# Kernel optimization log

Measured on AMD Instinct MI355X. Metric: run time of the kernel, lower is better.

The kernel has to match this reference:

```python
import jax, jax.numpy as jnp
import numpy as np
from jax.ops import segment_sum

N, E, F_IN, G, C = 20000, 640000, 128, 64, 2


def setup_inputs() -> dict:
    key = jax.random.key(0)
    ks = jax.random.split(key, 16)
    g = lambda k, s: (jax.random.normal(k, s, jnp.float32) * 0.05)
    z = lambda s: jnp.zeros(s, jnp.float32)
    inp = {
        'x': jax.random.normal(ks[0], (N, F_IN), jnp.float32),
        'edge_index': jax.random.randint(ks[1], (2, E), 0, N),
        'batch': jnp.sort(jax.random.randint(ks[2], (N,), 0, G)),
        'w1': g(ks[3], (F_IN, 64)), 'b1': z((64,)),
        'w2': g(ks[4], (64, 64)), 'b2': z((64,)),
        'w3': g(ks[5], (64, 128)), 'b3': z((128,)),
        'w4': g(ks[6], (128, 256)), 'b4': z((256,)),
        'lstm_wih': g(ks[7], (512, 256)), 'lstm_whh': g(ks[8], (512, 128)),
        'lstm_bih': z((512,)), 'lstm_bhh': z((512,)),
        'attn_in_w': g(ks[9], (384, 128)), 'attn_in_b': z((384,)),
        'attn_out_w': g(ks[10], (128, 128)), 'attn_out_b': z((128,)),
        'lin1_w': g(ks[11], (64, 128)), 'lin1_b': z((64,)),
        'lin2_w': g(ks[12], (C, 64)), 'lin2_b': z((C,)),
    }
    return inp


def _gcn(x, src, dst, norm, w, b):
    # PyG GCNConv: h = x @ W; out[dst] += norm_e * h[src]; + bias
    h = x @ w
    msg = h[src] * norm[:, None]
    return segment_sum(msg, dst, num_segments=N) + b


def forward(x, edge_index, batch, w1, b1, w2, b2, w3, b3, w4, b4,
            lstm_wih, lstm_whh, lstm_bih, lstm_bhh,
            attn_in_w, attn_in_b, attn_out_w, attn_out_b,
            lin1_w, lin1_b, lin2_w, lin2_b):
    # ---- GCN normalization with self-loops (shared across layers) ----
    loop = jnp.arange(N)
    src = jnp.concatenate([edge_index[0], loop])
    dst = jnp.concatenate([edge_index[1], loop])
    deg = segment_sum(jnp.ones_like(src, jnp.float32), dst, num_segments=N)
    dinv = jnp.where(deg > 0, jax.lax.rsqrt(deg), 0.0)
    norm = dinv[src] * dinv[dst]

    h = jax.nn.relu(_gcn(x, src, dst, norm, w1, b1))   # [N,64]  (dropout = eval no-op)
    h = jax.nn.relu(_gcn(h, src, dst, norm, w2, b2))   # [N,64]
    h = jax.nn.relu(_gcn(h, src, dst, norm, w3, b3))   # [N,128]
    h = jax.nn.relu(_gcn(h, src, dst, norm, w4, b4))   # [N,256]

    # ---- LSTM over the node sequence (batch 1, seq N), PyTorch gate order i,f,g,o ----
    xg = h @ lstm_wih.T + (lstm_bih + lstm_bhh)        # [N,512] precomputed input gates

    def step(carry, xg_t):
        hh, cc = carry
        gates = xg_t + lstm_whh @ hh                    # [512]
        i, f, gg, o = jnp.split(gates, 4)
        i, f, o = jax.nn.sigmoid(i), jax.nn.sigmoid(f), jax.nn.sigmoid(o)
        cc = f * cc + i * jnp.tanh(gg)
        hh = o * jnp.tanh(cc)
        return (hh, cc), hh

    init = (jnp.zeros(128, h.dtype), jnp.zeros(128, h.dtype))
    _, hs = jax.lax.scan(step, init, xg)               # [N,128]

    # ---- MultiheadAttention: input (L=1, B=N, E=128); softmax over length-1 seq ----
    qkv = hs @ attn_in_w.T + attn_in_b                 # [N,384]
    q, k, v = jnp.split(qkv, 3, axis=-1)
    qh = q.reshape(N, 8, 16); kh = k.reshape(N, 8, 16); vh = v.reshape(N, 8, 16)
    scores = jnp.sum(qh * kh, -1, keepdims=True) / 4.0  # [N,8,1], key dim = 1
    a = jax.nn.softmax(scores, axis=-1)                 # == 1 (single key)
    ctx = (a * vh).reshape(N, 128)
    attn = ctx @ attn_out_w.T + attn_out_b             # [N,128]

    # ---- global mean pool over graphs ----
    sums = segment_sum(attn, batch, num_segments=G)    # [G,128]
    cnt = segment_sum(jnp.ones(N, attn.dtype), batch, num_segments=G)
    pooled = sums / jnp.maximum(cnt, 1.0)[:, None]

    z1 = jax.nn.relu(pooled @ lin1_w.T + lin1_b)
    logits = z1 @ lin2_w.T + lin2_b                    # [G,C]
    return jax.nn.log_softmax(logits, axis=1)


def reference(x, edge_index, batch, w1, b1, w2, b2, w3, b3, w4, b4,
              lstm_wih, lstm_whh, lstm_bih, lstm_bhh,
              attn_in_w, attn_in_b, attn_out_w, attn_out_b,
              lin1_w, lin1_b, lin2_w, lin2_b):
    return forward(x, edge_index, batch, w1, b1, w2, b2, w3, b3, w4, b4,
                   lstm_wih, lstm_whh, lstm_bih, lstm_bhh,
                   attn_in_w, attn_in_b, attn_out_w, attn_out_b,
                   lin1_w, lin1_b, lin2_w, lin2_b)
```

## Files before the change

kernel.cpp:

```cpp
#include <hip/hip_runtime.h>
#include <cstdint>
#include <cstddef>

#define N_NODES 20000
#define N_EDGES 640000
#define N_GRAPH 64

typedef __attribute__((ext_vector_type(8))) short bf16x8;
typedef __attribute__((ext_vector_type(4))) float f32x4;

__device__ __forceinline__ float sigmoidf_(float x) {
    return 1.0f / (1.0f + __expf(-x));
}
__device__ __forceinline__ float tanhf_(float x) {
    float xc = fminf(fmaxf(x, -9.0f), 9.0f);
    float e = __expf(2.0f * xc);
    return (e - 1.0f) / (e + 1.0f);
}
__device__ __forceinline__ unsigned short f2bf_(float x) {
    unsigned int u = __builtin_bit_cast(unsigned int, x);
    return (unsigned short)((u + 0x7fffu + ((u >> 16) & 1u)) >> 16);
}

__global__ void count_kernel(const int* __restrict__ dst, int* __restrict__ cnt, int e) {
    int i = blockIdx.x * blockDim.x + threadIdx.x;
    if (i < e) atomicAdd(&cnt[dst[i]], 1);
}

__global__ void scan_kernel(const int* __restrict__ cnt, int* __restrict__ rowstart, int n) {
    __shared__ int buf[1024];
    __shared__ int carry_sh;
    int tid = threadIdx.x;
    if (tid == 0) carry_sh = 0;
    __syncthreads();
    for (int base = 0; base < n; base += 1024) {
        int i = base + tid;
        int v = (i < n) ? cnt[i] : 0;
        buf[tid] = v;
        __syncthreads();
        for (int off = 1; off < 1024; off <<= 1) {
            int t = (tid >= off) ? buf[tid - off] : 0;
            __syncthreads();
            buf[tid] += t;
            __syncthreads();
        }
        int carry = carry_sh;
        if (i < n) rowstart[i] = carry + buf[tid] - v;
        __syncthreads();
        if (tid == 1023) carry_sh = carry + buf[1023];
        __syncthreads();
    }
    if (tid == 0) rowstart[n] = carry_sh;
}

__global__ void dinv_kernel(const int* __restrict__ cnt, float* __restrict__ dinv, int n) {
    int i = blockIdx.x * blockDim.x + threadIdx.x;
    if (i < n) dinv[i] = rsqrtf((float)cnt[i] + 1.0f);
}

__global__ void fill_kernel(const int* __restrict__ src, const int* __restrict__ dst,
                            const int* __restrict__ rowstart, int* __restrict__ cursor,
                            int* __restrict__ csr_src, int e) {
    int i = blockIdx.x * blockDim.x + threadIdx.x;
    if (i < e) {
        int d = dst[i];
        int pos = rowstart[d] + atomicAdd(&cursor[d], 1);
        csr_src[pos] = src[i];
    }
}

template <bool BT, bool RELU, bool BIAS>
__global__ void gemm_kernel(const float* __restrict__ A, const float* __restrict__ B,
                            const float* __restrict__ bias, float* __restrict__ C,
                            int M, int K, int F) {
    __shared__ float As[16][65];
    __shared__ float Bs[16][65];
    int bm = blockIdx.x * 64;
    int bn = blockIdx.y * 64;
    int tid = threadIdx.x;
    int tm = (tid >> 4) << 2;
    int tn = (tid & 15) << 2;
    float acc[4][4] = {};
    for (int k0 = 0; k0 < K; k0 += 16) {
        {
            int idx = tid * 4;
            int m = idx >> 4;
            int kk = idx & 15;
            int gm = bm + m;
            float4 v = make_float4(0.f, 0.f, 0.f, 0.f);
            if (gm < M) v = *(const float4*)&A[(size_t)gm * K + k0 + kk];
            As[kk + 0][m] = v.x; As[kk + 1][m] = v.y; As[kk + 2][m] = v.z; As[kk + 3][m] = v.w;
        }
        if (BT) {
            int idx = tid * 4;
            int nn = idx >> 4;
            int kk = idx & 15;
            float4 v = *(const float4*)&B[(size_t)(bn + nn) * K + k0 + kk];
            Bs[kk + 0][nn] = v.x; Bs[kk + 1][nn] = v.y; Bs[kk + 2][nn] = v.z; Bs[kk + 3][nn] = v.w;
        } else {
            int idx = tid * 4;
            int kk = idx >> 6;
            int nn = idx & 63;
            float4 v = *(const float4*)&B[(size_t)(k0 + kk) * F + bn + nn];
            Bs[kk][nn + 0] = v.x; Bs[kk][nn + 1] = v.y; Bs[kk][nn + 2] = v.z; Bs[kk][nn + 3] = v.w;
        }
        __syncthreads();
#pragma unroll
        for (int kk = 0; kk < 16; ++kk) {
            float av[4], bv[4];
#pragma unroll
            for (int i = 0; i < 4; ++i) av[i] = As[kk][tm + i];
#pragma unroll
            for (int j = 0; j < 4; ++j) bv[j] = Bs[kk][tn + j];
#pragma unroll
            for (int i = 0; i < 4; ++i)
#pragma unroll
                for (int j = 0; j < 4; ++j) acc[i][j] += av[i] * bv[j];
        }
        __syncthreads();
    }
#pragma unroll
    for (int i = 0; i < 4; ++i) {
        int gm = bm + tm + i;
        if (gm >= M) continue;
#pragma unroll
        for (int j = 0; j < 4; ++j) {
            float v = acc[i][j];
            if (BIAS) v += bias[bn + tn + j];
            if (RELU) v = fmaxf(v, 0.0f);
            C[(size_t)gm * F + bn + tn + j] = v;
        }
    }
}

__global__ void agg_kernel(const float* __restrict__ H, const int* __restrict__ rowstart,
                           const int* __restrict__ csr_src, const float* __restrict__ dinv,
                           const float* __restrict__ bias, float* __restrict__ OUT, int F) {
    int n = blockIdx.x;
    int f = threadIdx.x;
    float di = dinv[n];
    int s = rowstart[n], e = rowstart[n + 1];
    float acc = di * H[(size_t)n * F + f];
    for (int i = s; i < e; ++i) {
        int src = csr_src[i];
        acc += dinv[src] * H[(size_t)src * F + f];
    }
    OUT[(size_t)n * F + f] = fmaxf(bias[f] + di * acc, 0.0f);
}

__global__ void vadd_kernel(const float* __restrict__ a, const float* __restrict__ b,
                            float* __restrict__ o, int n) {
    int i = blockIdx.x * blockDim.x + threadIdx.x;
    if (i < n) o[i] = a[i] + b[i];
}

__global__ void wprep_kernel(const float* __restrict__ whh, uint4* __restrict__ out) {
    int tau = blockIdx.x * blockDim.x + threadIdx.x;
    if (tau >= 8192) return;
    int l  = tau & 63;
    int f  = (tau >> 6) & 7;
    int w  = tau >> 9;
    int s  = f >> 2, kc = f & 3;
    int grow = 32 * w + 16 * s + (l & 15);
    int kb   = kc * 32 + (l >> 4) * 8;
    const float* src = whh + (size_t)grow * 128 + kb;
    unsigned int h[8];
#pragma unroll
    for (int j = 0; j < 8; ++j) h[j] = f2bf_(src[j]);
    uint4 v;
    v.x = h[0] | (h[1] << 16);
    v.y = h[2] | (h[3] << 16);
    v.z = h[4] | (h[5] << 16);
    v.w = h[6] | (h[7] << 16);
    out[tau] = v;
}

#define REP8(OP) OP(0) OP(1) OP(2) OP(3) OP(4) OP(5) OP(6) OP(7)

__global__ __launch_bounds__(1024)
__attribute__((amdgpu_waves_per_eu(4, 4)))
void lstm_mfma_kernel(const float* __restrict__ xg, const bf16x8* wfr,
                      const int* __restrict__ batch, float* poolsum, int steps) {
    __shared__ __align__(16) unsigned short h_bf[2][128];
    __shared__ __align__(16) float gates_s[512];
    const int t = threadIdx.x;
    const int w = t >> 6;
    const int l = t & 63;
    const int lg = l >> 4;
    const int rbase = 32 * w + 4 * lg;

#define AF(i) bf16x8 af##i = wfr[(size_t)(w * 8 + (i)) * 64 + l]; \
    asm volatile("" : "+v"(af##i));
    REP8(AF)
#undef AF

    if (t < 128) h_bf[0][t] = 0;
    float c = 0.0f, pacc = 0.0f;
    int curb = batch[0];
    f32x4 xc0 = *(const f32x4*)(xg + rbase);
    f32x4 xc1 = *(const f32x4*)(xg + rbase + 16);
    __syncthreads();

    int p = 0;
    for (int n = 0; n < steps; ++n) {
        bf16x8 b0 = *(const bf16x8*)&h_bf[p][ 0 + lg * 8];
        bf16x8 b1 = *(const bf16x8*)&h_bf[p][32 + lg * 8];
        bf16x8 b2 = *(const bf16x8*)&h_bf[p][64 + lg * 8];
        bf16x8 b3 = *(const bf16x8*)&h_bf[p][96 + lg * 8];

        const float* xp = xg + (size_t)((n + 1 < steps) ? n + 1 : n) * 512;
        f32x4 xn0 = *(const f32x4*)(xp + rbase);
        f32x4 xn1 = *(const f32x4*)(xp + rbase + 16);

        f32x4 a0 = xc0, a1 = xc1;
        a0 = __builtin_amdgcn_mfma_f32_16x16x32_bf16(af0, b0, a0, 0, 0, 0);
        a1 = __builtin_amdgcn_mfma_f32_16x16x32_bf16(af4, b0, a1, 0, 0, 0);
        a0 = __builtin_amdgcn_mfma_f32_16x16x32_bf16(af1, b1, a0, 0, 0, 0);
        a1 = __builtin_amdgcn_mfma_f32_16x16x32_bf16(af5, b1, a1, 0, 0, 0);
        a0 = __builtin_amdgcn_mfma_f32_16x16x32_bf16(af2, b2, a0, 0, 0, 0);
        a1 = __builtin_amdgcn_mfma_f32_16x16x32_bf16(af6, b2, a1, 0, 0, 0);
        a0 = __builtin_amdgcn_mfma_f32_16x16x32_bf16(af3, b3, a0, 0, 0, 0);
        a1 = __builtin_amdgcn_mfma_f32_16x16x32_bf16(af7, b3, a1, 0, 0, 0);

        if ((l & 15) == 0) {
            *(f32x4*)&gates_s[rbase]      = a0;
            *(f32x4*)&gates_s[rbase + 16] = a1;
        }
        __syncthreads();

        if (t < 128) {
            float iv = sigmoidf_(gates_s[t]);
            float fv = sigmoidf_(gates_s[t + 128]);
            float gg = tanhf_(gates_s[t + 256]);
            float ov = sigmoidf_(gates_s[t + 384]);
            c = fv * c + iv * gg;
            float hn = ov * tanhf_(c);
            h_bf[p ^ 1][t] = f2bf_(hn);
            int b = batch[n];
            if (b != curb) { poolsum[curb * 128 + t] = pacc; pacc = 0.0f; curb = b; }
            pacc += hn;
        }
        __syncthreads();

        xc0 = xn0; xc1 = xn1; p ^= 1;
    }
    if (t < 128) poolsum[curb * 128 + t] = pacc;
}

__global__ void head_kernel(const float* __restrict__ poolsum, const int* __restrict__ batch,
                            int nn,
                            const float* __restrict__ attn_in_w, const float* __restrict__ attn_in_b,
                            const float* __restrict__ attn_out_w, const float* __restrict__ attn_out_b,
                            const float* __restrict__ l1w, const float* __restrict__ l1b,
                            const float* __restrict__ l2w, const float* __restrict__ l2b,
                            float* __restrict__ out) {
    __shared__ float hbar[128], tv[128], pl[128], z1[64], lg[2];
    int g = blockIdx.x, t = threadIdx.x;
    int lo = 0, hi = nn;
    while (lo < hi) { int m = (lo + hi) >> 1; if (batch[m] < g) lo = m + 1; else hi = m; }
    int s0 = lo;
    lo = 0; hi = nn;
    while (lo < hi) { int m = (lo + hi) >> 1; if (batch[m] <= g) lo = m + 1; else hi = m; }
    int e0 = lo;
    float cntv = fmaxf((float)(e0 - s0), 1.0f);
    hbar[t] = poolsum[g * 128 + t] / cntv;
    __syncthreads();
    float a = attn_in_b[256 + t];
    for (int k = 0; k < 128; ++k) a += attn_in_w[(256 + t) * 128 + k] * hbar[k];
    tv[t] = a;
    __syncthreads();
    float pv = attn_out_b[t];
    for (int k = 0; k < 128; ++k) pv += attn_out_w[t * 128 + k] * tv[k];
    pl[t] = pv;
    __syncthreads();
    if (t < 64) {
        float z = l1b[t];
        for (int k = 0; k < 128; ++k) z += l1w[t * 128 + k] * pl[k];
        z1[t] = fmaxf(z, 0.0f);
    }
    __syncthreads();
    if (t < 2) {
        float lv = l2b[t];
        for (int k = 0; k < 64; ++k) lv += l2w[t * 64 + k] * z1[k];
        lg[t] = lv;
    }
    __syncthreads();
    if (t == 0) {
        float m = fmaxf(lg[0], lg[1]);
        float ls = m + logf(__expf(lg[0] - m) + __expf(lg[1] - m));
        out[g * 2 + 0] = lg[0] - ls;
        out[g * 2 + 1] = lg[1] - ls;
    }
}

extern "C" void kernel_launch(void* const* d_in, const int* in_sizes, int n_in,
                              void* d_out, int out_size, void* d_ws, size_t ws_size,
                              hipStream_t stream) {
    const float* x          = (const float*)d_in[0];
    const int*   ei         = (const int*)d_in[1];
    const int*   batch      = (const int*)d_in[2];
    const float* w1 = (const float*)d_in[3];  const float* b1 = (const float*)d_in[4];
    const float* w2 = (const float*)d_in[5];  const float* b2 = (const float*)d_in[6];
    const float* w3 = (const float*)d_in[7];  const float* b3 = (const float*)d_in[8];
    const float* w4 = (const float*)d_in[9];  const float* b4 = (const float*)d_in[10];
    const float* wih = (const float*)d_in[11]; const float* whh = (const float*)d_in[12];
    const float* bih = (const float*)d_in[13]; const float* bhh = (const float*)d_in[14];
    const float* attn_in_w  = (const float*)d_in[15]; const float* attn_in_b  = (const float*)d_in[16];
    const float* attn_out_w = (const float*)d_in[17]; const float* attn_out_b = (const float*)d_in[18];
    const float* l1w = (const float*)d_in[19]; const float* l1b = (const float*)d_in[20];
    const float* l2w = (const float*)d_in[21]; const float* l2b = (const float*)d_in[22];
    float* out = (float*)d_out;

    char* p = (char*)d_ws;
    auto alloc = [&](size_t bytes) {
        char* r = p;
        p += (bytes + 255) & ~(size_t)255;
        return r;
    };
    int*   cnt      = (int*)alloc((size_t)N_NODES * 4);
    int*   cursor   = (int*)alloc((size_t)N_NODES * 4);
    int*   rowstart = (int*)alloc((size_t)(N_NODES + 1) * 4);
    float* dinv     = (float*)alloc((size_t)N_NODES * 4);
    int*   csr      = (int*)alloc((size_t)N_EDGES * 4);
    float* bsum     = (float*)alloc(512 * 4);
    float* poolsum  = (float*)alloc((size_t)N_GRAPH * 128 * 4);
    uint4* wfrag    = (uint4*)alloc((size_t)8192 * 16);
    float* bufA     = (float*)alloc((size_t)N_NODES * 256 * 4);
    float* bufB     = (float*)alloc((size_t)N_NODES * 256 * 4);
    float* xg       = (float*)alloc((size_t)N_NODES * 512 * 4);

    hipMemsetAsync(cnt, 0, (size_t)N_NODES * 4, stream);
    hipMemsetAsync(cursor, 0, (size_t)N_NODES * 4, stream);
    hipMemsetAsync(poolsum, 0, (size_t)N_GRAPH * 128 * 4, stream);

    const int* srcp = ei;
    const int* dstp = ei + N_EDGES;

    int eb = (N_EDGES + 255) / 256;
    int nb = (N_NODES + 255) / 256;
    count_kernel<<<eb, 256, 0, stream>>>(dstp, cnt, N_EDGES);
    scan_kernel<<<1, 1024, 0, stream>>>(cnt, rowstart, N_NODES);
    dinv_kernel<<<nb, 256, 0, stream>>>(cnt, dinv, N_NODES);
    fill_kernel<<<eb, 256, 0, stream>>>(srcp, dstp, rowstart, cursor, csr, N_EDGES);
    wprep_kernel<<<32, 256, 0, stream>>>(whh, wfrag);

    int mg = (N_NODES + 63) / 64;
    gemm_kernel<false, false, false><<<dim3(mg, 1), 256, 0, stream>>>(x, w1, nullptr, bufA, N_NODES, 128, 64);
    agg_kernel<<<N_NODES, 64, 0, stream>>>(bufA, rowstart, csr, dinv, b1, bufB, 64);
    gemm_kernel<false, false, false><<<dim3(mg, 1), 256, 0, stream>>>(bufB, w2, nullptr, bufA, N_NODES, 64, 64);
    agg_kernel<<<N_NODES, 64, 0, stream>>>(bufA, rowstart, csr, dinv, b2, bufB, 64);
    gemm_kernel<false, false, false><<<dim3(mg, 2), 256, 0, stream>>>(bufB, w3, nullptr, bufA, N_NODES, 64, 128);
    agg_kernel<<<N_NODES, 128, 0, stream>>>(bufA, rowstart, csr, dinv, b3, bufB, 128);
    gemm_kernel<false, false, false><<<dim3(mg, 4), 256, 0, stream>>>(bufB, w4, nullptr, bufA, N_NODES, 128, 256);
    agg_kernel<<<N_NODES, 256, 0, stream>>>(bufA, rowstart, csr, dinv, b4, bufB, 256);

    vadd_kernel<<<2, 256, 0, stream>>>(bih, bhh, bsum, 512);
    gemm_kernel<true, false, true><<<dim3(mg, 8), 256, 0, stream>>>(bufB, wih, bsum, xg, N_NODES, 256, 512);

    lstm_mfma_kernel<<<1, 1024, 0, stream>>>(xg, (const bf16x8*)wfrag, batch, poolsum, N_NODES);

    head_kernel<<<N_GRAPH, 128, 0, stream>>>(poolsum, batch, N_NODES,
                                             attn_in_w, attn_in_b, attn_out_w, attn_out_b,
                                             l1w, l1b, l2w, l2b, out);
}
```

Measured before the change: 15.10 ms.

## Halve LSTM block to 8 waves holding weight fragments in AGPRs via inline asm

The sequential LSTM kernel now runs with 512 threads (8 waves) instead of 1024. Each wave computes 64 gate rows, so it needs four MFMA accumulator chains and 16 weight fragments, which are pinned in accumulation registers with v_accvgpr_write and used by hand-written MFMA asm. The input-gate contribution xg is no longer the MFMA accumulator seed. It is added afterwards by the 128 activation threads, which also prefetch the next step's values. The aim is to cut per-step barrier cost and wave count on the latency-bound recurrence. The risks are manual hazard handling (s_nop padding), clobbered AGPRs the compiler cannot see, and a longer MFMA dependency chain per wave.

```diff
diff --git a/kernel.cpp b/kernel.cpp
--- a/kernel.cpp
+++ b/kernel.cpp
@@ -158,10 +158,10 @@
     int tau = blockIdx.x * blockDim.x + threadIdx.x;
     if (tau >= 8192) return;
     int l  = tau & 63;
-    int f  = (tau >> 6) & 7;
-    int w  = tau >> 9;
+    int f  = (tau >> 6) & 15;
+    int w  = tau >> 10;
     int s  = f >> 2, kc = f & 3;
-    int grow = 32 * w + 16 * s + (l & 15);
+    int grow = 64 * w + 16 * s + (l & 15);
     int kb   = kc * 32 + (l >> 4) * 8;
     const float* src = whh + (size_t)grow * 128 + kb;
     unsigned int h[8];
@@ -175,30 +175,38 @@
     out[tau] = v;
 }
 
-#define REP8(OP) OP(0) OP(1) OP(2) OP(3) OP(4) OP(5) OP(6) OP(7)
-
-__global__ __launch_bounds__(1024)
-__attribute__((amdgpu_waves_per_eu(4, 4)))
-void lstm_mfma_kernel(const float* __restrict__ xg, const bf16x8* wfr,
-                      const int* __restrict__ batch, float* poolsum, int steps) {
+#define SF(i, A0, A1, A2, A3) { \
+    uint4 q = wfr[(size_t)(w * 16 + (i)) * 64 + l]; \
+    asm volatile("v_accvgpr_write_b32 a" #A0 ", %0\n\t" \
+                 "v_accvgpr_write_b32 a" #A1 ", %1\n\t" \
+                 "v_accvgpr_write_b32 a" #A2 ", %2\n\t" \
+                 "v_accvgpr_write_b32 a" #A3 ", %3" \
+                 :: "v"(q.x), "v"(q.y), "v"(q.z), "v"(q.w) \
+                 : "a" #A0, "a" #A1, "a" #A2, "a" #A3); }
+
+__global__ __launch_bounds__(512)
+void lstm_mfma_kernel(const float* __restrict__ xg, const uint4* __restrict__ wfr,
+                      const int* __restrict__ batch, float* __restrict__ poolsum, int steps) {
     __shared__ __align__(16) unsigned short h_bf[2][128];
     __shared__ __align__(16) float gates_s[512];
     const int t = threadIdx.x;
     const int w = t >> 6;
     const int l = t & 63;
     const int lg = l >> 4;
-    const int rbase = 32 * w + 4 * lg;
-
-#define AF(i) bf16x8 af##i = wfr[(size_t)(w * 8 + (i)) * 64 + l]; \
-    asm volatile("" : "+v"(af##i));
-    REP8(AF)
-#undef AF
+
+    SF(0, 0, 1, 2, 3)     SF(1, 4, 5, 6, 7)     SF(2, 8, 9, 10, 11)    SF(3, 12, 13, 14, 15)
+    SF(4, 16, 17, 18, 19) SF(5, 20, 21, 22, 23) SF(6, 24, 25, 26, 27)  SF(7, 28, 29, 30, 31)
+    SF(8, 32, 33, 34, 35) SF(9, 36, 37, 38, 39) SF(10, 40, 41, 42, 43) SF(11, 44, 45, 46, 47)
+    SF(12, 48, 49, 50, 51) SF(13, 52, 53, 54, 55) SF(14, 56, 57, 58, 59) SF(15, 60, 61, 62, 63)
 
     if (t < 128) h_bf[0][t] = 0;
     float c = 0.0f, pacc = 0.0f;
-    int curb = batch[0];
-    f32x4 xc0 = *(const f32x4*)(xg + rbase);
-    f32x4 xc1 = *(const f32x4*)(xg + rbase + 16);
+    int curb = 0;
+    float x0 = 0.f, x1 = 0.f, x2 = 0.f, x3 = 0.f;
+    if (t < 128) {
+        curb = batch[0];
+        x0 = xg[t]; x1 = xg[t + 128]; x2 = xg[t + 256]; x3 = xg[t + 384];
+    }
     __syncthreads();
 
     int p = 0;
@@ -208,31 +216,53 @@
         bf16x8 b2 = *(const bf16x8*)&h_bf[p][64 + lg * 8];
         bf16x8 b3 = *(const bf16x8*)&h_bf[p][96 + lg * 8];
 
-        const float* xp = xg + (size_t)((n + 1 < steps) ? n + 1 : n) * 512;
-        f32x4 xn0 = *(const f32x4*)(xp + rbase);
-        f32x4 xn1 = *(const f32x4*)(xp + rbase + 16);
-
-        f32x4 a0 = xc0, a1 = xc1;
-        a0 = __builtin_amdgcn_mfma_f32_16x16x32_bf16(af0, b0, a0, 0, 0, 0);
-        a1 = __builtin_amdgcn_mfma_f32_16x16x32_bf16(af4, b0, a1, 0, 0, 0);
-        a0 = __builtin_amdgcn_mfma_f32_16x16x32_bf16(af1, b1, a0, 0, 0, 0);
-        a1 = __builtin_amdgcn_mfma_f32_16x16x32_bf16(af5, b1, a1, 0, 0, 0);
-        a0 = __builtin_amdgcn_mfma_f32_16x16x32_bf16(af2, b2, a0, 0, 0, 0);
-        a1 = __builtin_amdgcn_mfma_f32_16x16x32_bf16(af6, b2, a1, 0, 0, 0);
-        a0 = __builtin_amdgcn_mfma_f32_16x16x32_bf16(af3, b3, a0, 0, 0, 0);
-        a1 = __builtin_amdgcn_mfma_f32_16x16x32_bf16(af7, b3, a1, 0, 0, 0);
+        f32x4 a0 = {0.f, 0.f, 0.f, 0.f}, a1 = a0, a2 = a0, a3 = a0;
+        asm volatile(
+            "s_nop 1\n\t"
+            "v_mfma_f32_16x16x32_bf16 %0, a[0:3],   %4, %0\n\t"
+            "v_mfma_f32_16x16x32_bf16 %1, a[16:19], %4, %1\n\t"
+            "v_mfma_f32_16x16x32_bf16 %2, a[32:35], %4, %2\n\t"
+            "v_mfma_f32_16x16x32_bf16 %3, a[48:51], %4, %3"
+            : "+v"(a0), "+v"(a1), "+v"(a2), "+v"(a3) : "v"(b0));
+        asm volatile(
+            "v_mfma_f32_16x16x32_bf16 %0, a[4:7],   %4, %0\n\t"
+            "v_mfma_f32_16x16x32_bf16 %1, a[20:23], %4, %1\n\t"
+            "v_mfma_f32_16x16x32_bf16 %2, a[36:39], %4, %2\n\t"
+            "v_mfma_f32_16x16x32_bf16 %3, a[52:55], %4, %3"
+            : "+v"(a0), "+v"(a1), "+v"(a2), "+v"(a3) : "v"(b1));
+        asm volatile(
+            "v_mfma_f32_16x16x32_bf16 %0, a[8:11],  %4, %0\n\t"
+            "v_mfma_f32_16x16x32_bf16 %1, a[24:27], %4, %1\n\t"
+            "v_mfma_f32_16x16x32_bf16 %2, a[40:43], %4, %2\n\t"
+            "v_mfma_f32_16x16x32_bf16 %3, a[56:59], %4, %3"
+            : "+v"(a0), "+v"(a1), "+v"(a2), "+v"(a3) : "v"(b2));
+        asm volatile(
+            "v_mfma_f32_16x16x32_bf16 %0, a[12:15], %4, %0\n\t"
+            "v_mfma_f32_16x16x32_bf16 %1, a[28:31], %4, %1\n\t"
+            "v_mfma_f32_16x16x32_bf16 %2, a[44:47], %4, %2\n\t"
+            "v_mfma_f32_16x16x32_bf16 %3, a[60:63], %4, %3\n\t"
+            "s_nop 7\n\t"
+            "s_nop 7"
+            : "+v"(a0), "+v"(a1), "+v"(a2), "+v"(a3) : "v"(b3));
 
         if ((l & 15) == 0) {
-            *(f32x4*)&gates_s[rbase]      = a0;
-            *(f32x4*)&gates_s[rbase + 16] = a1;
+            int base = 64 * w + 4 * lg;
+            *(f32x4*)&gates_s[base]      = a0;
+            *(f32x4*)&gates_s[base + 16] = a1;
+            *(f32x4*)&gates_s[base + 32] = a2;
+            *(f32x4*)&gates_s[base + 48] = a3;
         }
         __syncthreads();
 
         if (t < 128) {
-            float iv = sigmoidf_(gates_s[t]);
-            float fv = sigmoidf_(gates_s[t + 128]);
-            float gg = tanhf_(gates_s[t + 256]);
-            float ov = sigmoidf_(gates_s[t + 384]);
+            float iv = sigmoidf_(gates_s[t]       + x0);
+            float fv = sigmoidf_(gates_s[t + 128] + x1);
+            float gg = tanhf_   (gates_s[t + 256] + x2);
+            float ov = sigmoidf_(gates_s[t + 384] + x3);
+            if (n + 1 < steps) {
+                const float* xp = xg + (size_t)(n + 1) * 512;
+                x0 = xp[t]; x1 = xp[t + 128]; x2 = xp[t + 256]; x3 = xp[t + 384];
+            }
             c = fv * c + iv * gg;
             float hn = ov * tanhf_(c);
             h_bf[p ^ 1][t] = f2bf_(hn);
@@ -241,8 +271,7 @@
             pacc += hn;
         }
         __syncthreads();
-
-        xc0 = xn0; xc1 = xn1; p ^= 1;
+        p ^= 1;
     }
     if (t < 128) poolsum[curb * 128 + t] = pacc;
 }
@@ -357,7 +386,7 @@
     vadd_kernel<<<2, 256, 0, stream>>>(bih, bhh, bsum, 512);
     gemm_kernel<true, false, true><<<dim3(mg, 8), 256, 0, stream>>>(bufB, wih, bsum, xg, N_NODES, 256, 512);
 
-    lstm_mfma_kernel<<<1, 1024, 0, stream>>>(xg, (const bf16x8*)wfrag, batch, poolsum, N_NODES);
+    lstm_mfma_kernel<<<1, 512, 0, stream>>>(xg, (const uint4*)wfrag, batch, poolsum, N_NODES);
 
     head_kernel<<<N_GRAPH, 128, 0, stream>>>(poolsum, batch, N_NODES,
                                              attn_in_w, attn_in_b, attn_out_w, attn_out_b,
```

New measurement: 16.22 ms. +7.4%, slower.
